# Kernel tuning notes

Hardware: AMD Instinct MI355X
Metric: run time of the kernel (lower is better)

The kernel has to match this reference:

```python
import jax, jax.numpy as jnp
import numpy as np

N = 50000          # number of nodes
NNZ = 800000       # edges per relation (avg degree 16)
R = 3              # edge_features / number of relations
D_IN = 128
D_OUT = 128
EPS = 1e-6


def setup_inputs() -> dict:
    key = jax.random.key(0)
    ks = jax.random.split(key, 8)
    return {
        "input": jax.random.normal(ks[0], (N, D_IN), dtype=jnp.float32),
        "adj_rows": jax.random.randint(ks[1], (R, NNZ), 0, N, dtype=jnp.int64) if jax.config.jax_enable_x64 else jax.random.randint(ks[1], (R, NNZ), 0, N).astype(jnp.int32),
        "adj_cols": jax.random.randint(ks[2], (R, NNZ), 0, N, dtype=jnp.int64) if jax.config.jax_enable_x64 else jax.random.randint(ks[2], (R, NNZ), 0, N).astype(jnp.int32),
        "adj_vals": jax.random.uniform(ks[3], (R, NNZ), dtype=jnp.float32),
        "weight": jax.random.normal(ks[4], (D_IN * R, D_OUT), dtype=jnp.float32) * (1.0 / np.sqrt(D_OUT)),
        "share_weight": jax.random.normal(ks[5], (D_IN, D_OUT), dtype=jnp.float32) * (1.0 / np.sqrt(D_OUT)),
        "bias": jax.random.normal(ks[6], (D_OUT,), dtype=jnp.float32) * (1.0 / np.sqrt(D_OUT)),
        "ln_gamma": jnp.ones((D_IN,), dtype=jnp.float32),
        "ln_beta": jnp.zeros((D_IN,), dtype=jnp.float32),
    }


def _spmm(rows, cols, vals, x, n_nodes):
    # (sparse A) @ x via gather + segment-sum: out[r] = sum_{e: rows[e]=r} vals[e]*x[cols[e]]
    msgs = vals[:, None] * x[cols]            # [nnz, d]
    return jax.ops.segment_sum(msgs, rows, num_segments=n_nodes)


def _layernorm(x, gamma, beta):
    mu = jnp.mean(x, axis=-1, keepdims=True)
    var = jnp.var(x, axis=-1, keepdims=True)
    return (x - mu) * jax.lax.rsqrt(var + EPS) * gamma + beta


def reference(input, adj_rows, adj_cols, adj_vals, weight, share_weight, bias, ln_gamma, ln_beta):
    n = input.shape[0]
    # loop over the small fixed relation set to keep peak memory low
    support_list = [
        _spmm(adj_rows[r], adj_cols[r], adj_vals[r], input, n) for r in range(adj_rows.shape[0])
    ]
    support = jnp.concatenate(support_list, axis=1)   # [N, R*d_in]
    support_sum = support_list[0]
    for s in support_list[1:]:
        support_sum = support_sum + s
    support_norm = _layernorm(support_sum, ln_gamma, ln_beta)
    out = (support @ weight + support_norm @ share_weight) * 0.5
    return out + bias
```

## Files before the change

### kernel.cpp

```cpp
#include <hip/hip_runtime.h>

constexpr int NN  = 50000;
constexpr int NNZ = 800000;
constexpr int RR  = 3;
constexpr int D   = 128;
constexpr int RN  = RR * NN;
constexpr int NE  = RR * NNZ;
constexpr int KK  = 512;
constexpr int MPAD = 50048;
constexpr int PART = 256;
constexpr int PSZ  = (RN + PART - 1) / PART;
constexpr int CAP  = 10240;
constexpr int EPB  = 2048;
constexpr int CAPB = 24;
constexpr float EPS = 1e-6f;

using bf16x8 = __attribute__((ext_vector_type(8))) __bf16;
using f32x4  = __attribute__((ext_vector_type(4))) float;

__device__ __forceinline__ unsigned pack_bf2(float a, float b) {
  unsigned ua = __float_as_uint(a); ua = (ua + (0x7FFFu + ((ua >> 16) & 1))) >> 16;
  unsigned ub = __float_as_uint(b); ub = (ub + (0x7FFFu + ((ub >> 16) & 1))) >> 16;
  return ua | (ub << 16);
}
__device__ __forceinline__ unsigned bf16_lo(float a) {
  unsigned ua = __float_as_uint(a);
  return (ua + (0x7FFFu + ((ua >> 16) & 1))) >> 16;
}

__device__ __forceinline__ void gload16(const void* g, void* l) {
  __builtin_amdgcn_global_load_lds(
      (const __attribute__((address_space(1))) unsigned int*)g,
      (__attribute__((address_space(3))) unsigned int*)l, 16, 0, 0);
}

__global__ __launch_bounds__(256) void part_split(
    const int*   __restrict__ rows,
    const int*   __restrict__ cols,
    const float* __restrict__ vals,
    int* __restrict__ pcur,
    uint2* __restrict__ pedges) {
  __shared__ int lcur[PART], lbase[PART];
  __shared__ uint2 lbuf[PART][CAPB];
  int t = threadIdx.x;
  lcur[t] = 0;
  __syncthreads();
  int e0 = blockIdx.x * EPB;
  constexpr int EPT = EPB / 256;
  int ovf_pe[EPT], ovf_rank[EPT];
  uint2 ovf_val[EPT];
  #pragma unroll
  for (int j = 0; j < EPT; j++) {
    ovf_pe[j] = -1;
    int e = e0 + j * 256 + t;
    if (e < NE) {
      int r = (e >= 2 * NNZ) ? 2 : (e >= NNZ ? 1 : 0);
      int b = r * NN + rows[e];
      int p = b / PSZ;
      unsigned pay = ((unsigned)cols[e] << 16) | bf16_lo(vals[e]);
      int rank = atomicAdd(&lcur[p], 1);
      if (rank < CAPB) {
        lbuf[p][rank] = make_uint2((unsigned)b, pay);
      } else {
        ovf_pe[j] = p; ovf_rank[j] = rank;
        ovf_val[j] = make_uint2((unsigned)b, pay);
      }
    }
  }
  __syncthreads();
  lbase[t] = atomicAdd(&pcur[t], lcur[t]);
  __syncthreads();
  int wid = t >> 6, l = t & 63;
  for (int q = 0; q < 64; q++) {
    int p = wid * 64 + q;
    int n = min(lcur[p], CAPB);
    uint2* dst = pedges + (size_t)p * CAP + lbase[p];
    for (int i = l; i < n; i += 64) dst[i] = lbuf[p][i];
  }
  #pragma unroll
  for (int j = 0; j < EPT; j++)
    if (ovf_pe[j] >= 0)
      pedges[(size_t)ovf_pe[j] * CAP + lbase[ovf_pe[j]] + ovf_rank[j]] = ovf_val[j];
}

__global__ __launch_bounds__(64) void psum(
    const int* __restrict__ pcur, int* __restrict__ pbase, int* __restrict__ off) {
  int l = threadIdx.x;
  int carry = 0;
  for (int base = 0; base < PART; base += 64) {
    int v = pcur[base + l];
    int inc = v;
    #pragma unroll
    for (int s = 1; s < 64; s <<= 1) {
      int u = __shfl_up(inc, s);
      if (l >= s) inc += u;
    }
    pbase[base + l] = inc - v + carry;
    carry += __shfl(inc, 63);
  }
  if (l == 0) off[RN] = NE;
}

__global__ __launch_bounds__(256) void sort_part(
    const uint2* __restrict__ pedges,
    const int*   __restrict__ pcur,
    const int*   __restrict__ pbase,
    int* __restrict__ off,
    unsigned* __restrict__ epack) {
  __shared__ int sc[PSZ];
  __shared__ int sdata[256];
  int p = blockIdx.x;
  int t = threadIdx.x;
  int bb = p * PSZ;
  int nbuck = min(PSZ, RN - bb);
  int n = pcur[p];
  int gbase = pbase[p];
  const uint2* src = pedges + (size_t)p * CAP;

  for (int i = t; i < nbuck; i += 256) sc[i] = 0;
  __syncthreads();
  for (int i = t; i < n; i += 256)
    atomicAdd(&sc[src[i].x - bb], 1);
  __syncthreads();

  constexpr int PER = (PSZ + 255) / 256;
  int lo = t * PER, hi = min(lo + PER, nbuck);
  int s = 0;
  for (int i = lo; i < hi; i++) s += sc[i];
  sdata[t] = s;
  __syncthreads();
  #pragma unroll
  for (int step = 1; step < 256; step <<= 1) {
    int v = (t >= step) ? sdata[t - step] : 0;
    __syncthreads();
    sdata[t] += v;
    __syncthreads();
  }
  int run = gbase + sdata[t] - s;
  for (int i = lo; i < hi; i++) {
    int c = sc[i];
    sc[i] = run;
    off[bb + i] = run;
    run += c;
  }
  __syncthreads();

  for (int i = t; i < n; i += 256) {
    uint2 ed = src[i];
    int pos = atomicAdd(&sc[ed.x - bb], 1);
    epack[pos] = ed.y;
  }
}

__global__ __launch_bounds__(256) void build_xb(
    const float* __restrict__ x, unsigned* __restrict__ xb) {
  int i = blockIdx.x * 256 + threadIdx.x;
  if (i >= NN * 64) return;
  float2 v = ((const float2*)x)[i];
  xb[i] = pack_bf2(v.x, v.y);
}

__global__ __launch_bounds__(256) void gather_ln(
    const unsigned* __restrict__ xb,
    const unsigned* __restrict__ epack,
    const int*      __restrict__ off,
    const float* __restrict__ gamma,
    const float* __restrict__ beta,
    unsigned* __restrict__ Au) {
  int node = blockIdx.x * 4 + (threadIdx.x >> 6);
  if (node >= NN) return;
  int l = threadIdx.x & 63;
  float2 tot = make_float2(0.f, 0.f);
  #pragma unroll
  for (int r = 0; r < RR; r++) {
    int b = r * NN + node;
    int s = off[b], e2 = off[b + 1];
    float2 acc = make_float2(0.f, 0.f);
    int i = s;
    for (; i + 8 <= e2; i += 8) {
      unsigned u0 = epack[i + 0], u1 = epack[i + 1];
      unsigned u2 = epack[i + 2], u3 = epack[i + 3];
      unsigned u4 = epack[i + 4], u5 = epack[i + 5];
      unsigned u6 = epack[i + 6], u7 = epack[i + 7];
      unsigned g0 = xb[(u0 >> 16) * 64 + l];
      unsigned g1 = xb[(u1 >> 16) * 64 + l];
      unsigned g2 = xb[(u2 >> 16) * 64 + l];
      unsigned g3 = xb[(u3 >> 16) * 64 + l];
      unsigned g4 = xb[(u4 >> 16) * 64 + l];
      unsigned g5 = xb[(u5 >> 16) * 64 + l];
      unsigned g6 = xb[(u6 >> 16) * 64 + l];
      unsigned g7 = xb[(u7 >> 16) * 64 + l];
      float v0 = __uint_as_float(u0 << 16), v1 = __uint_as_float(u1 << 16);
      float v2 = __uint_as_float(u2 << 16), v3 = __uint_as_float(u3 << 16);
      float v4 = __uint_as_float(u4 << 16), v5 = __uint_as_float(u5 << 16);
      float v6 = __uint_as_float(u6 << 16), v7 = __uint_as_float(u7 << 16);
      acc.x += v0 * __uint_as_float(g0 << 16) + v1 * __uint_as_float(g1 << 16)
             + v2 * __uint_as_float(g2 << 16) + v3 * __uint_as_float(g3 << 16)
             + v4 * __uint_as_float(g4 << 16) + v5 * __uint_as_float(g5 << 16)
             + v6 * __uint_as_float(g6 << 16) + v7 * __uint_as_float(g7 << 16);
      acc.y += v0 * __uint_as_float(g0 & 0xFFFF0000u) + v1 * __uint_as_float(g1 & 0xFFFF0000u)
             + v2 * __uint_as_float(g2 & 0xFFFF0000u) + v3 * __uint_as_float(g3 & 0xFFFF0000u)
             + v4 * __uint_as_float(g4 & 0xFFFF0000u) + v5 * __uint_as_float(g5 & 0xFFFF0000u)
             + v6 * __uint_as_float(g6 & 0xFFFF0000u) + v7 * __uint_as_float(g7 & 0xFFFF0000u);
    }
    for (; i < e2; i++) {
      unsigned u = epack[i];
      unsigned g = xb[(u >> 16) * 64 + l];
      float v = __uint_as_float(u << 16);
      acc.x += v * __uint_as_float(g << 16);
      acc.y += v * __uint_as_float(g & 0xFFFF0000u);
    }
    Au[(size_t)node * 256 + r * 64 + l] = pack_bf2(acc.x, acc.y);
    tot.x += acc.x;
    tot.y += acc.y;
  }
  float sum = tot.x + tot.y;
  float sq  = tot.x * tot.x + tot.y * tot.y;
  #pragma unroll
  for (int m = 32; m >= 1; m >>= 1) {
    sum += __shfl_xor(sum, m);
    sq  += __shfl_xor(sq,  m);
  }
  float mean = sum * (1.0f / D);
  float var  = sq * (1.0f / D) - mean * mean;
  float rstd = rsqrtf(var + EPS);
  int d = l * 2;
  float o0 = (tot.x - mean) * rstd * gamma[d]     + beta[d];
  float o1 = (tot.y - mean) * rstd * gamma[d + 1] + beta[d + 1];
  Au[(size_t)node * 256 + 192 + l] = pack_bf2(o0, o1);
}

__global__ __launch_bounds__(256) void build_wt(
    const float* __restrict__ w,
    const float* __restrict__ shw,
    unsigned short* __restrict__ WT) {
  int idx = blockIdx.x * 256 + threadIdx.x;
  int k   = idx >> 7;
  int col = idx & 127;
  float v = (k < 384) ? w[k * 128 + col] : shw[(k - 384) * 128 + col];
  WT[col * 512 + k] = (unsigned short)bf16_lo(v);
}

__global__ __launch_bounds__(256) void gemm_mfma(
    const char* __restrict__ Ab,
    const char* __restrict__ Bb,
    const float* __restrict__ bias,
    float* __restrict__ out) {
  __shared__ __align__(16) char smem[24576];
  char* As = smem;
  char* Bs = smem + 8192;

  int tid  = threadIdx.x;
  int wid  = tid >> 6;
  int lane = tid & 63;
  int wr   = wid >> 1;
  int wc   = wid & 1;
  int row0 = blockIdx.x * 64;

  f32x4 zero = {0.f, 0.f, 0.f, 0.f};
  f32x4 acc[2][4];
  #pragma unroll
  for (int i = 0; i < 2; i++)
    #pragma unroll
    for (int j = 0; j < 4; j++) acc[i][j] = zero;

  for (int kc = 0; kc < 8; kc++) {
    #pragma unroll
    for (int i = 0; i < 2; i++) {
      int c = i * 256 + tid;
      int r = c >> 3, s = c & 7;
      int ss = s ^ (r & 7);
      const void* src = Ab + (size_t)(row0 + r) * 1024 + kc * 128 + ss * 16;
      void* dst = As + i * 4096 + wid * 1024;
      gload16(src, dst);
    }
    #pragma unroll
    for (int i = 0; i < 4; i++) {
      int c = i * 256 + tid;
      int r = c >> 3, s = c & 7;
      int ss = s ^ (r & 7);
      const void* src = Bb + (size_t)r * 1024 + kc * 128 + ss * 16;
      void* dst = Bs + i * 4096 + wid * 1024;
      gload16(src, dst);
    }
    __syncthreads();

    #pragma unroll
    for (int ks = 0; ks < 2; ks++) {
      bf16x8 afrag[2], bfrag[4];
      int sg = ks * 4 + (lane >> 4);
      #pragma unroll
      for (int rb = 0; rb < 2; rb++) {
        int r = wr * 32 + rb * 16 + (lane & 15);
        afrag[rb] = *(const bf16x8*)(As + r * 128 + (sg ^ (r & 7)) * 16);
      }
      #pragma unroll
      for (int cb = 0; cb < 4; cb++) {
        int col = wc * 64 + cb * 16 + (lane & 15);
        bfrag[cb] = *(const bf16x8*)(Bs + col * 128 + (sg ^ (col & 7)) * 16);
      }
      #pragma unroll
      for (int rb = 0; rb < 2; rb++)
        #pragma unroll
        for (int cb = 0; cb < 4; cb++)
          acc[rb][cb] = __builtin_amdgcn_mfma_f32_16x16x32_bf16(
              afrag[rb], bfrag[cb], acc[rb][cb], 0, 0, 0);
    }
    __syncthreads();
  }

  #pragma unroll
  for (int rb = 0; rb < 2; rb++) {
    #pragma unroll
    for (int cb = 0; cb < 4; cb++) {
      int col = wc * 64 + cb * 16 + (lane & 15);
      float bv = bias[col];
      #pragma unroll
      for (int r = 0; r < 4; r++) {
        int grow = row0 + wr * 32 + rb * 16 + (lane >> 4) * 4 + r;
        if (grow < NN) out[(size_t)grow * 128 + col] = 0.5f * acc[rb][cb][r] + bv;
      }
    }
  }
}

extern "C" void kernel_launch(void* const* d_in, const int* in_sizes, int n_in,
                              void* d_out, int out_size, void* d_ws, size_t ws_size,
                              hipStream_t stream) {
  const float* input  = (const float*)d_in[0];
  const int*   arows  = (const int*)  d_in[1];
  const int*   acols  = (const int*)  d_in[2];
  const float* avals  = (const float*)d_in[3];
  const float* weight = (const float*)d_in[4];
  const float* shw    = (const float*)d_in[5];
  const float* bias   = (const float*)d_in[6];
  const float* gamma  = (const float*)d_in[7];
  const float* beta   = (const float*)d_in[8];
  float* out = (float*)d_out;

  char* ws = (char*)d_ws;
  char*  Abf   = ws;                         ws += (size_t)MPAD * KK * 2;
  unsigned short* WT = (unsigned short*)ws;  ws += (size_t)128 * KK * 2;
  unsigned* xb  = (unsigned*)ws;             ws += (size_t)NN * 64 * 4;
  uint2* pedges = (uint2*)ws;                ws += (size_t)PART * CAP * sizeof(uint2);
  unsigned* epack = (unsigned*)ws;           ws += (size_t)NE * 4;
  int*   off   = (int*)ws;                   ws += ((size_t)RN + 4) * sizeof(int);
  int*   pcur  = (int*)ws;                   ws += (size_t)PART * sizeof(int);
  int*   pbase = (int*)ws;                   ws += (size_t)PART * sizeof(int);

  hipMemsetAsync(pcur, 0, (size_t)PART * sizeof(int), stream);
  build_wt   <<<256, 256, 0, stream>>>(weight, shw, WT);
  build_xb   <<<(NN * 64 + 255) / 256, 256, 0, stream>>>(input, xb);
  part_split <<<(NE + EPB - 1) / EPB, 256, 0, stream>>>(arows, acols, avals,
                                                        pcur, pedges);
  psum       <<<1, 64, 0, stream>>>(pcur, pbase, off);
  sort_part  <<<PART, 256, 0, stream>>>(pedges, pcur, pbase, off, epack);
  gather_ln  <<<(NN + 3) / 4, 256, 0, stream>>>(xb, epack, off, gamma, beta,
                                                (unsigned*)Abf);
  gemm_mfma  <<<MPAD / 64, 256, 0, stream>>>(Abf, (const char*)WT, bias, out);
}
```

Baseline: 207.2 us.

## Gather with 16-byte row loads, four edges per wave and shuffle-broadcast indices

The gather+layernorm kernel now splits each wave into four groups of 16 lanes. Each group handles a different edge and each lane loads a 16-byte chunk of the bf16 source row, so one wave fetches four rows at once. Edge descriptors are loaded coalesced, one per lane, then broadcast with shuffles, and the per-group partial sums are combined with xor-shuffles before a vectorized store. This aims to cut the number of load instructions and raise memory-level parallelism, at the cost of extra shuffles and idle lanes on the tail of each node's edge list.

After: 185.7 us. 10.4% less time.

```diff
diff --git a/kernel.cpp b/kernel.cpp
--- a/kernel.cpp
+++ b/kernel.cpp
@@ -27,6 +27,8 @@
   unsigned ua = __float_as_uint(a);
   return (ua + (0x7FFFu + ((ua >> 16) & 1))) >> 16;
 }
+__device__ __forceinline__ float blo(unsigned u) { return __uint_as_float(u << 16); }
+__device__ __forceinline__ float bhi(unsigned u) { return __uint_as_float(u & 0xFFFF0000u); }
 
 __device__ __forceinline__ void gload16(const void* g, void* l) {
   __builtin_amdgcn_global_load_lds(
@@ -169,65 +171,90 @@
     unsigned* __restrict__ Au) {
   int node = blockIdx.x * 4 + (threadIdx.x >> 6);
   if (node >= NN) return;
-  int l = threadIdx.x & 63;
-  float2 tot = make_float2(0.f, 0.f);
+  int lane = threadIdx.x & 63;
+  int g  = lane >> 4;
+  int q  = lane & 15;
+  int q4 = q * 4;
+
+  float l0=0,l1=0,l2=0,l3=0,l4=0,l5=0,l6=0,l7=0;
+
   #pragma unroll
   for (int r = 0; r < RR; r++) {
     int b = r * NN + node;
     int s = off[b], e2 = off[b + 1];
-    float2 acc = make_float2(0.f, 0.f);
-    int i = s;
-    for (; i + 8 <= e2; i += 8) {
-      unsigned u0 = epack[i + 0], u1 = epack[i + 1];
-      unsigned u2 = epack[i + 2], u3 = epack[i + 3];
-      unsigned u4 = epack[i + 4], u5 = epack[i + 5];
-      unsigned u6 = epack[i + 6], u7 = epack[i + 7];
-      unsigned g0 = xb[(u0 >> 16) * 64 + l];
-      unsigned g1 = xb[(u1 >> 16) * 64 + l];
-      unsigned g2 = xb[(u2 >> 16) * 64 + l];
-      unsigned g3 = xb[(u3 >> 16) * 64 + l];
-      unsigned g4 = xb[(u4 >> 16) * 64 + l];
-      unsigned g5 = xb[(u5 >> 16) * 64 + l];
-      unsigned g6 = xb[(u6 >> 16) * 64 + l];
-      unsigned g7 = xb[(u7 >> 16) * 64 + l];
-      float v0 = __uint_as_float(u0 << 16), v1 = __uint_as_float(u1 << 16);
-      float v2 = __uint_as_float(u2 << 16), v3 = __uint_as_float(u3 << 16);
-      float v4 = __uint_as_float(u4 << 16), v5 = __uint_as_float(u5 << 16);
-      float v6 = __uint_as_float(u6 << 16), v7 = __uint_as_float(u7 << 16);
-      acc.x += v0 * __uint_as_float(g0 << 16) + v1 * __uint_as_float(g1 << 16)
-             + v2 * __uint_as_float(g2 << 16) + v3 * __uint_as_float(g3 << 16)
-             + v4 * __uint_as_float(g4 << 16) + v5 * __uint_as_float(g5 << 16)
-             + v6 * __uint_as_float(g6 << 16) + v7 * __uint_as_float(g7 << 16);
-      acc.y += v0 * __uint_as_float(g0 & 0xFFFF0000u) + v1 * __uint_as_float(g1 & 0xFFFF0000u)
-             + v2 * __uint_as_float(g2 & 0xFFFF0000u) + v3 * __uint_as_float(g3 & 0xFFFF0000u)
-             + v4 * __uint_as_float(g4 & 0xFFFF0000u) + v5 * __uint_as_float(g5 & 0xFFFF0000u)
-             + v6 * __uint_as_float(g6 & 0xFFFF0000u) + v7 * __uint_as_float(g7 & 0xFFFF0000u);
-    }
-    for (; i < e2; i++) {
-      unsigned u = epack[i];
-      unsigned g = xb[(u >> 16) * 64 + l];
-      float v = __uint_as_float(u << 16);
-      acc.x += v * __uint_as_float(g << 16);
-      acc.y += v * __uint_as_float(g & 0xFFFF0000u);
-    }
-    Au[(size_t)node * 256 + r * 64 + l] = pack_bf2(acc.x, acc.y);
-    tot.x += acc.x;
-    tot.y += acc.y;
-  }
-  float sum = tot.x + tot.y;
-  float sq  = tot.x * tot.x + tot.y * tot.y;
-  #pragma unroll
-  for (int m = 32; m >= 1; m >>= 1) {
+    float a0=0,a1=0,a2=0,a3=0,a4=0,a5=0,a6=0,a7=0;
+
+    for (int i0 = s; i0 < e2; i0 += 64) {
+      int navail = min(64, e2 - i0);
+      unsigned ep = (lane < navail) ? epack[i0 + lane] : 0u;
+      int c0 = 0;
+      for (; c0 + 8 <= navail; c0 += 8) {
+        unsigned ua = __shfl(ep, c0 + g);
+        unsigned ub = __shfl(ep, c0 + 4 + g);
+        uint4 ga = *(const uint4*)(xb + (size_t)(ua >> 16) * 64 + q4);
+        uint4 gb = *(const uint4*)(xb + (size_t)(ub >> 16) * 64 + q4);
+        float va = blo(ua), vb = blo(ub);
+        a0 += va * blo(ga.x); a1 += va * bhi(ga.x);
+        a2 += va * blo(ga.y); a3 += va * bhi(ga.y);
+        a4 += va * blo(ga.z); a5 += va * bhi(ga.z);
+        a6 += va * blo(ga.w); a7 += va * bhi(ga.w);
+        a0 += vb * blo(gb.x); a1 += vb * bhi(gb.x);
+        a2 += vb * blo(gb.y); a3 += vb * bhi(gb.y);
+        a4 += vb * blo(gb.z); a5 += vb * bhi(gb.z);
+        a6 += vb * blo(gb.w); a7 += vb * bhi(gb.w);
+      }
+      for (; c0 < navail; c0 += 4) {
+        int eidx = c0 + g;
+        unsigned u = __shfl(ep, min(eidx, navail - 1));
+        float v = (eidx < navail) ? blo(u) : 0.0f;
+        uint4 gg = *(const uint4*)(xb + (size_t)(u >> 16) * 64 + q4);
+        a0 += v * blo(gg.x); a1 += v * bhi(gg.x);
+        a2 += v * blo(gg.y); a3 += v * bhi(gg.y);
+        a4 += v * blo(gg.z); a5 += v * bhi(gg.z);
+        a6 += v * blo(gg.w); a7 += v * bhi(gg.w);
+      }
+    }
+    #define REDG(x) x += __shfl_xor(x, 16); x += __shfl_xor(x, 32);
+    REDG(a0) REDG(a1) REDG(a2) REDG(a3) REDG(a4) REDG(a5) REDG(a6) REDG(a7)
+    #undef REDG
+    if (g == 0) {
+      uint4 w;
+      w.x = pack_bf2(a0, a1); w.y = pack_bf2(a2, a3);
+      w.z = pack_bf2(a4, a5); w.w = pack_bf2(a6, a7);
+      *(uint4*)(Au + (size_t)node * 256 + r * 64 + q4) = w;
+    }
+    l0 += a0; l1 += a1; l2 += a2; l3 += a3;
+    l4 += a4; l5 += a5; l6 += a6; l7 += a7;
+  }
+
+  float sum = l0+l1+l2+l3+l4+l5+l6+l7;
+  float sq  = l0*l0+l1*l1+l2*l2+l3*l3+l4*l4+l5*l5+l6*l6+l7*l7;
+  #pragma unroll
+  for (int m = 1; m <= 8; m <<= 1) {
     sum += __shfl_xor(sum, m);
     sq  += __shfl_xor(sq,  m);
   }
   float mean = sum * (1.0f / D);
   float var  = sq * (1.0f / D) - mean * mean;
   float rstd = rsqrtf(var + EPS);
-  int d = l * 2;
-  float o0 = (tot.x - mean) * rstd * gamma[d]     + beta[d];
-  float o1 = (tot.y - mean) * rstd * gamma[d + 1] + beta[d + 1];
-  Au[(size_t)node * 256 + 192 + l] = pack_bf2(o0, o1);
+  float4 gm0 = *(const float4*)&gamma[8 * q];
+  float4 gm1 = *(const float4*)&gamma[8 * q + 4];
+  float4 bt0 = *(const float4*)&beta[8 * q];
+  float4 bt1 = *(const float4*)&beta[8 * q + 4];
+  float o0 = (l0 - mean) * rstd * gm0.x + bt0.x;
+  float o1 = (l1 - mean) * rstd * gm0.y + bt0.y;
+  float o2 = (l2 - mean) * rstd * gm0.z + bt0.z;
+  float o3 = (l3 - mean) * rstd * gm0.w + bt0.w;
+  float o4 = (l4 - mean) * rstd * gm1.x + bt1.x;
+  float o5 = (l5 - mean) * rstd * gm1.y + bt1.y;
+  float o6 = (l6 - mean) * rstd * gm1.z + bt1.z;
+  float o7 = (l7 - mean) * rstd * gm1.w + bt1.w;
+  if (g == 0) {
+    uint4 w;
+    w.x = pack_bf2(o0, o1); w.y = pack_bf2(o2, o3);
+    w.z = pack_bf2(o4, o5); w.w = pack_bf2(o6, o7);
+    *(uint4*)(Au + (size_t)node * 256 + 192 + q4) = w;
+  }
 }
 
 __global__ __launch_bounds__(256) void build_wt(
```
